# Optimization experiments

Hardware: AMD Instinct MI355X
Metric: run time of the kernel (lower is better)

The kernel has to match this reference:

```python
import jax, jax.numpy as jnp
import numpy as np

N_NODES = 100000
N_EDGES = 1000000
D = 64
N_LAYERS = 3
BATCH = 4096


def setup_inputs() -> dict:
    key = jax.random.key(0)
    ks = jax.random.split(key, 12)
    inp = {
        "embeds": jax.random.normal(ks[0], (N_NODES, D), dtype=jnp.float32) * 0.1,
        "edge_weight": jax.random.uniform(ks[1], (N_EDGES,), dtype=jnp.float32),
        "W_gc": jax.random.normal(ks[2], (N_LAYERS, D, D), dtype=jnp.float32) * 0.1,
        "b_gc": jax.random.normal(ks[3], (N_LAYERS, 1, D), dtype=jnp.float32) * 0.1,
        "W_bi": jax.random.normal(ks[4], (N_LAYERS, D, D), dtype=jnp.float32) * 0.1,
        "b_bi": jax.random.normal(ks[5], (N_LAYERS, 1, D), dtype=jnp.float32) * 0.1,
        "edge_index": jax.random.randint(ks[6], (2, N_EDGES), 0, N_NODES, dtype=jnp.int64) if jax.config.jax_enable_x64 else jax.random.randint(ks[6], (2, N_EDGES), 0, N_NODES, dtype=jnp.int32),
        "users": jax.random.randint(ks[7], (BATCH,), 0, 50000, dtype=jnp.int32),
        "pos_items": jax.random.randint(ks[8], (BATCH,), 0, N_NODES, dtype=jnp.int32),
        "neg_items": jax.random.randint(ks[9], (BATCH,), 0, N_NODES, dtype=jnp.int32),
    }
    return inp


def _l2_normalize(x, eps=1e-12):
    # matches torch F.normalize(p=2, dim=1): divide by clamped norm
    n = jnp.sqrt(jnp.sum(x * x, axis=1, keepdims=True))
    return x / jnp.maximum(n, eps)


def reference(embeds, edge_weight, W_gc, b_gc, W_bi, b_bi, edge_index, users, pos_items, neg_items):
    row, col = edge_index[0], edge_index[1]
    n_nodes = embeds.shape[0]
    ego = embeds
    all_embeddings = [ego]
    for k in range(W_gc.shape[0]):
        # gather-scale-scatter graph aggregation
        msgs = ego[row] * edge_weight[:, None]                     # [E, D]
        side = jax.ops.segment_sum(msgs, col, num_segments=n_nodes)  # [N, D]
        sum_emb = side @ W_gc[k] + b_gc[k]                          # [N, D]
        bi_emb = (ego * side) @ W_bi[k] + b_bi[k]                   # [N, D]
        ego = jax.nn.leaky_relu(sum_emb + bi_emb, negative_slope=0.2)
        all_embeddings.append(_l2_normalize(ego))
    all_embeddings = jnp.concatenate(all_embeddings, axis=1)        # [N, 4*D]
    user_embs = all_embeddings[users]
    pos_item_embs = all_embeddings[pos_items]
    neg_item_embs = all_embeddings[neg_items]
    return (user_embs, pos_item_embs, neg_item_embs, user_embs, pos_item_embs, neg_item_embs)
```

## Files before the change

### kernel.cpp

```cpp
#include <hip/hip_runtime.h>

#define NN 100000
#define NE 1000000
#define DD 64
#define NB 4096
#define TILE 1024
#define NTILE ((NN + TILE - 1) / TILE)

__global__ __launch_bounds__(256) void k_count(
    const int* __restrict__ ei, int* __restrict__ base, int* __restrict__ rank)
{
  const int stride = gridDim.x * blockDim.x;
  for (int e = blockIdx.x * blockDim.x + threadIdx.x; e < NE; e += stride)
    rank[e] = atomicAdd(&base[ei[NE + e]], 1);
}

__global__ __launch_bounds__(256) void k_scan_part(
    const int* __restrict__ base, int* __restrict__ tilesum)
{
  __shared__ int s[256];
  const int t = threadIdx.x;
  const int i0 = blockIdx.x * TILE + t * 4;
  int4 v = make_int4(0, 0, 0, 0);
  if (i0 < NN) v = *reinterpret_cast<const int4*>(base + i0);
  s[t] = v.x + v.y + v.z + v.w;
  __syncthreads();
#pragma unroll
  for (int off = 128; off >= 1; off >>= 1) {
    if (t < off) s[t] += s[t + off];
    __syncthreads();
  }
  if (t == 0) tilesum[blockIdx.x] = s[0];
}

__global__ __launch_bounds__(128) void k_scan_tiles(
    const int* __restrict__ tilesum, int* __restrict__ tileoff)
{
  __shared__ int s[128];
  const int t = threadIdx.x;
  const int v = (t < NTILE) ? tilesum[t] : 0;
  s[t] = v;
  __syncthreads();
#pragma unroll
  for (int off = 1; off < 128; off <<= 1) {
    const int u = (t >= off) ? s[t - off] : 0;
    __syncthreads();
    s[t] += u;
    __syncthreads();
  }
  if (t < NTILE) tileoff[t] = s[t] - v;
}

__global__ __launch_bounds__(256) void k_scan_apply(
    int* __restrict__ base, const int* __restrict__ tileoff)
{
  __shared__ int s[256];
  const int t = threadIdx.x;
  const int i0 = blockIdx.x * TILE + t * 4;
  int4 v = make_int4(0, 0, 0, 0);
  if (i0 < NN) v = *reinterpret_cast<const int4*>(base + i0);
  const int sum = v.x + v.y + v.z + v.w;
  s[t] = sum;
  __syncthreads();
#pragma unroll
  for (int off = 1; off < 256; off <<= 1) {
    const int u = (t >= off) ? s[t - off] : 0;
    __syncthreads();
    s[t] += u;
    __syncthreads();
  }
  int p = s[t] - sum + tileoff[blockIdx.x];
  if (i0 < NN) {
    const int4 o = make_int4(p, p + v.x, p + v.x + v.y, p + v.x + v.y + v.z);
    *reinterpret_cast<int4*>(base + i0) = o;
  }
  if (blockIdx.x == 0 && t == 0) base[NN] = NE;
}

__global__ __launch_bounds__(256) void k_permute(
    const int* __restrict__ ei, const float* __restrict__ ew,
    const int* __restrict__ base, const int* __restrict__ rank,
    int2* __restrict__ edata)
{
  const int stride = gridDim.x * blockDim.x;
  for (int e = blockIdx.x * blockDim.x + threadIdx.x; e < NE; e += stride) {
    const int c = ei[NE + e];
    const int slot = base[c] + rank[e];
    edata[slot] = make_int2(ei[e], __float_as_int(ew[e]));
  }
}

__global__ __launch_bounds__(256) void k_aggregate(
    const float* __restrict__ ego, const int* __restrict__ base,
    const int2* __restrict__ edata, float* __restrict__ side)
{
  const int lane = threadIdx.x & 63;
  const int gw = (blockIdx.x * 256 + threadIdx.x) >> 6;
  const int nw = (gridDim.x * 256) >> 6;
  for (int n = gw; n < NN; n += nw) {
    const int lo = base[n];
    const int hi = base[n + 1];
    float acc = 0.f;
    int j = lo;
    for (; j + 3 < hi; j += 4) {
      const int2 a = edata[j];
      const int2 b = edata[j + 1];
      const int2 c = edata[j + 2];
      const int2 d = edata[j + 3];
      const float va = ego[(size_t)a.x * DD + lane];
      const float vb = ego[(size_t)b.x * DD + lane];
      const float vc = ego[(size_t)c.x * DD + lane];
      const float vd = ego[(size_t)d.x * DD + lane];
      acc = fmaf(va, __int_as_float(a.y), acc);
      acc = fmaf(vb, __int_as_float(b.y), acc);
      acc = fmaf(vc, __int_as_float(c.y), acc);
      acc = fmaf(vd, __int_as_float(d.y), acc);
    }
    for (; j < hi; ++j) {
      const int2 a = edata[j];
      acc = fmaf(ego[(size_t)a.x * DD + lane], __int_as_float(a.y), acc);
    }
    side[(size_t)n * DD + lane] = acc;
  }
}

__global__ __launch_bounds__(256) void k_update(
    const float* __restrict__ side, const float* __restrict__ ego_in,
    float* __restrict__ ego_out, float* __restrict__ normed,
    const float* __restrict__ Wgc, const float* __restrict__ bgc,
    const float* __restrict__ Wbi, const float* __restrict__ bbi)
{
  const int lane = threadIdx.x & 63;
  float wg[DD], wb[DD];
#pragma unroll
  for (int j = 0; j < DD; ++j) {
    wg[j] = Wgc[j * DD + lane];
    wb[j] = Wbi[j * DD + lane];
  }
  const float bias = bgc[lane] + bbi[lane];
  const int gw = (blockIdx.x * 256 + threadIdx.x) >> 6;
  const int nw = (gridDim.x * 256) >> 6;
  for (int n = gw; n < NN; n += nw) {
    const float s = side[(size_t)n * DD + lane];
    const float e = ego_in[(size_t)n * DD + lane];
    const float p = s * e;
    float ag = 0.f, ab = 0.f;
#pragma unroll
    for (int j = 0; j < DD; ++j) {
      const float sj = __uint_as_float(__builtin_amdgcn_readlane(__float_as_uint(s), j));
      const float pj = __uint_as_float(__builtin_amdgcn_readlane(__float_as_uint(p), j));
      ag = fmaf(sj, wg[j], ag);
      ab = fmaf(pj, wb[j], ab);
    }
    float x = ag + ab + bias;
    x = (x > 0.f) ? x : 0.2f * x;
    ego_out[(size_t)n * DD + lane] = x;
    float ss = x * x;
#pragma unroll
    for (int off = 32; off >= 1; off >>= 1) ss += __shfl_xor(ss, off);
    const float nrm = fmaxf(sqrtf(ss), 1e-12f);
    normed[(size_t)n * DD + lane] = x / nrm;
  }
}

__global__ __launch_bounds__(256) void k_gather(
    const float* __restrict__ src, const int* __restrict__ users,
    const int* __restrict__ pos, const int* __restrict__ neg,
    float* __restrict__ out, int colOff)
{
  const int w = (blockIdx.x * 256 + threadIdx.x) >> 6;
  const int lane = threadIdx.x & 63;
  if (w >= 3 * NB) return;
  const int t = w / NB;
  const int i = w - t * NB;
  const int* idxp = (t == 0) ? users : ((t == 1) ? pos : neg);
  const int idx = idxp[i];
  const float v = src[(size_t)idx * DD + lane];
  const size_t o = (size_t)w * 256 + colOff + lane;
  out[o] = v;
  out[o + (size_t)3 * NB * 256] = v;
}

extern "C" void kernel_launch(void* const* d_in, const int* in_sizes, int n_in,
                              void* d_out, int out_size, void* d_ws, size_t ws_size,
                              hipStream_t stream)
{
  const float* embeds = (const float*)d_in[0];
  const float* ew     = (const float*)d_in[1];
  const float* Wgc    = (const float*)d_in[2];
  const float* bgc    = (const float*)d_in[3];
  const float* Wbi    = (const float*)d_in[4];
  const float* bbi    = (const float*)d_in[5];
  const int*   ei     = (const int*)d_in[6];
  const int*   users  = (const int*)d_in[7];
  const int*   pos    = (const int*)d_in[8];
  const int*   neg    = (const int*)d_in[9];
  float* out = (float*)d_out;

  float* side = (float*)d_ws;
  float* ego  = side + (size_t)NN * DD;
  float* norm = ego  + (size_t)NN * DD;
  int*   base   = (int*)(norm + (size_t)NN * DD);
  int*   tiles  = base + (NN + 4);
  int2*  edata  = (int2*)(tiles + 2 * ((NTILE + 1) & ~1));
  int*   rank = (int*)side;

  const dim3 blk(256);

  k_gather<<<dim3((3 * NB) / 4), blk, 0, stream>>>(embeds, users, pos, neg, out, 0);

  hipMemsetAsync(base, 0, (size_t)(NN + 4) * sizeof(int), stream);
  k_count<<<dim3(4096), blk, 0, stream>>>(ei, base, rank);
  k_scan_part<<<dim3(NTILE), blk, 0, stream>>>(base, tiles);
  k_scan_tiles<<<dim3(1), dim3(128), 0, stream>>>(tiles, tiles + ((NTILE + 1) & ~1));
  k_scan_apply<<<dim3(NTILE), blk, 0, stream>>>(base, tiles + ((NTILE + 1) & ~1));
  k_permute<<<dim3(4096), blk, 0, stream>>>(ei, ew, base, rank, edata);

  const float* cur = embeds;
  for (int k = 0; k < 3; ++k) {
    k_aggregate<<<dim3(4096), blk, 0, stream>>>(cur, base, edata, side);
    k_update<<<dim3(2048), blk, 0, stream>>>(
        side, cur, ego, norm,
        Wgc + (size_t)k * DD * DD, bgc + (size_t)k * DD,
        Wbi + (size_t)k * DD * DD, bbi + (size_t)k * DD);
    k_gather<<<dim3((3 * NB) / 4), blk, 0, stream>>>(norm, users, pos, neg, out,
                                                     DD * (k + 1));
    cur = ego;
  }
}
```

Measured before the change: 489.9 us.

## Defer L2 normalization to batch gather and fuse ego*side product into aggregation

```diff
diff --git a/kernel.cpp b/kernel.cpp
--- a/kernel.cpp
+++ b/kernel.cpp
@@ -90,9 +90,10 @@
   }
 }
 
-__global__ __launch_bounds__(256) void k_aggregate(
+__global__ __launch_bounds__(256) void k_aggregate2(
     const float* __restrict__ ego, const int* __restrict__ base,
-    const int2* __restrict__ edata, float* __restrict__ side)
+    const int2* __restrict__ edata, float* __restrict__ side,
+    float* __restrict__ prod)
 {
   const int lane = threadIdx.x & 63;
   const int gw = (blockIdx.x * 256 + threadIdx.x) >> 6;
@@ -100,6 +101,7 @@
   for (int n = gw; n < NN; n += nw) {
     const int lo = base[n];
     const int hi = base[n + 1];
+    const float eg = ego[(size_t)n * DD + lane];
     float acc = 0.f;
     int j = lo;
     for (; j + 3 < hi; j += 4) {
@@ -121,12 +123,13 @@
       acc = fmaf(ego[(size_t)a.x * DD + lane], __int_as_float(a.y), acc);
     }
     side[(size_t)n * DD + lane] = acc;
-  }
-}
-
-__global__ __launch_bounds__(256) void k_update(
-    const float* __restrict__ side, const float* __restrict__ ego_in,
-    float* __restrict__ ego_out, float* __restrict__ normed,
+    prod[(size_t)n * DD + lane] = acc * eg;
+  }
+}
+
+__global__ __launch_bounds__(256) void k_update4(
+    const float* __restrict__ side, const float* __restrict__ prod,
+    float* __restrict__ ego_out,
     const float* __restrict__ Wgc, const float* __restrict__ bgc,
     const float* __restrict__ Wbi, const float* __restrict__ bbi)
 {
@@ -140,26 +143,19 @@
   const float bias = bgc[lane] + bbi[lane];
   const int gw = (blockIdx.x * 256 + threadIdx.x) >> 6;
   const int nw = (gridDim.x * 256) >> 6;
+#pragma unroll 1
   for (int n = gw; n < NN; n += nw) {
-    const float s = side[(size_t)n * DD + lane];
-    const float e = ego_in[(size_t)n * DD + lane];
-    const float p = s * e;
-    float ag = 0.f, ab = 0.f;
+    const int nu = __builtin_amdgcn_readfirstlane(n);
+    const float* __restrict__ srow = side + (size_t)nu * DD;
+    const float* __restrict__ prow = prod + (size_t)nu * DD;
+    float acc = bias;
 #pragma unroll
     for (int j = 0; j < DD; ++j) {
-      const float sj = __uint_as_float(__builtin_amdgcn_readlane(__float_as_uint(s), j));
-      const float pj = __uint_as_float(__builtin_amdgcn_readlane(__float_as_uint(p), j));
-      ag = fmaf(sj, wg[j], ag);
-      ab = fmaf(pj, wb[j], ab);
+      acc = fmaf(srow[j], wg[j], acc);
+      acc = fmaf(prow[j], wb[j], acc);
     }
-    float x = ag + ab + bias;
-    x = (x > 0.f) ? x : 0.2f * x;
-    ego_out[(size_t)n * DD + lane] = x;
-    float ss = x * x;
-#pragma unroll
-    for (int off = 32; off >= 1; off >>= 1) ss += __shfl_xor(ss, off);
-    const float nrm = fmaxf(sqrtf(ss), 1e-12f);
-    normed[(size_t)n * DD + lane] = x / nrm;
+    const float x = (acc > 0.f) ? acc : 0.2f * acc;
+    ego_out[(size_t)nu * DD + lane] = x;
   }
 }
 
@@ -179,6 +175,29 @@
   const size_t o = (size_t)w * 256 + colOff + lane;
   out[o] = v;
   out[o + (size_t)3 * NB * 256] = v;
+}
+
+__global__ __launch_bounds__(256) void k_gather_norm(
+    const float* __restrict__ src, const int* __restrict__ users,
+    const int* __restrict__ pos, const int* __restrict__ neg,
+    float* __restrict__ out, int colOff)
+{
+  const int w = (blockIdx.x * 256 + threadIdx.x) >> 6;
+  const int lane = threadIdx.x & 63;
+  if (w >= 3 * NB) return;
+  const int t = w / NB;
+  const int i = w - t * NB;
+  const int* idxp = (t == 0) ? users : ((t == 1) ? pos : neg);
+  const int idx = idxp[i];
+  const float v = src[(size_t)idx * DD + lane];
+  float ss = v * v;
+#pragma unroll
+  for (int off = 32; off >= 1; off >>= 1) ss += __shfl_xor(ss, off);
+  const float nrm = fmaxf(sqrtf(ss), 1e-12f);
+  const float nv = v / nrm;
+  const size_t o = (size_t)w * 256 + colOff + lane;
+  out[o] = nv;
+  out[o + (size_t)3 * NB * 256] = nv;
 }
 
 extern "C" void kernel_launch(void* const* d_in, const int* in_sizes, int n_in,
@@ -199,8 +218,8 @@
 
   float* side = (float*)d_ws;
   float* ego  = side + (size_t)NN * DD;
-  float* norm = ego  + (size_t)NN * DD;
-  int*   base   = (int*)(norm + (size_t)NN * DD);
+  float* prod = ego  + (size_t)NN * DD;
+  int*   base   = (int*)(prod + (size_t)NN * DD);
   int*   tiles  = base + (NN + 4);
   int2*  edata  = (int2*)(tiles + 2 * ((NTILE + 1) & ~1));
   int*   rank = (int*)side;
@@ -218,13 +237,13 @@
 
   const float* cur = embeds;
   for (int k = 0; k < 3; ++k) {
-    k_aggregate<<<dim3(4096), blk, 0, stream>>>(cur, base, edata, side);
-    k_update<<<dim3(2048), blk, 0, stream>>>(
-        side, cur, ego, norm,
+    k_aggregate2<<<dim3(4096), blk, 0, stream>>>(cur, base, edata, side, prod);
+    k_update4<<<dim3(1024), blk, 0, stream>>>(
+        side, prod, ego,
         Wgc + (size_t)k * DD * DD, bgc + (size_t)k * DD,
         Wbi + (size_t)k * DD * DD, bbi + (size_t)k * DD);
-    k_gather<<<dim3((3 * NB) / 4), blk, 0, stream>>>(norm, users, pos, neg, out,
-                                                     DD * (k + 1));
+    k_gather_norm<<<dim3((3 * NB) / 4), blk, 0, stream>>>(ego, users, pos, neg, out,
+                                                          DD * (k + 1));
     cur = ego;
   }
 }
```

Measured after the change: 516.8 us. 1.05x slower.
